# Kernel optimization log

Measured on AMD Instinct MI355X. Metric: run time of the kernel, lower is better.

Reference implementation:

```python
import jax, jax.numpy as jnp
import numpy as np

B, S, E, H = 1, 4096, 768, 12
D = E // H  # head_dim = 64


def setup_inputs() -> dict:
    key = jax.random.key(0)
    ks = jax.random.split(key, 9)
    s = 1.0 / np.sqrt(E)
    return {
        "x": jax.random.normal(ks[0], (B, S, E), dtype=jnp.float32),
        "Wq": jax.random.uniform(ks[1], (E, E), jnp.float32, -s, s),
        "bq": jax.random.uniform(ks[2], (E,), jnp.float32, -s, s),
        "Wk": jax.random.uniform(ks[3], (E, E), jnp.float32, -s, s),
        "bk": jax.random.uniform(ks[4], (E,), jnp.float32, -s, s),
        "Wv": jax.random.uniform(ks[5], (E, E), jnp.float32, -s, s),
        "bv": jax.random.uniform(ks[6], (E,), jnp.float32, -s, s),
        "Wo": jax.random.uniform(ks[7], (E, E), jnp.float32, -s, s),
        "bo": jax.random.uniform(ks[8], (E,), jnp.float32, -s, s),
    }


def reference(x, Wq, bq, Wk, bk, Wv, bv, Wo, bo):
    b, s, e = x.shape
    # QKV projections, split heads -> [b, h, s, d]
    def split(t):
        return t.reshape(b, s, H, D).transpose(0, 2, 1, 3)
    q = split(x @ Wq.T + bq)
    k = split(x @ Wk.T + bk)
    v = split(x @ Wv.T + bv)
    scores = jnp.einsum("bhqd,bhkd->bhqk", q, k) / jnp.sqrt(jnp.float32(D))
    attn = jax.nn.softmax(scores, axis=-1)  # dropout is identity in eval
    out = jnp.einsum("bhqk,bhkd->bhqd", attn, v)
    out = out.transpose(0, 2, 1, 3).reshape(b, s, e)
    return out @ Wo.T + bo
```

## Files before the change

kernel.cpp:

```cpp
#include <hip/hip_runtime.h>
#include <hip/hip_bf16.h>
#include <math.h>

#define SEQ 4096
#define EDIM 768
#define NHEAD 12
#define HDIM 64
#define SE (SEQ * EDIM)
#define WMAT (EDIM * EDIM)
#define QSCALE 0.180336880111f

typedef __attribute__((ext_vector_type(8))) __bf16 bf16x8;
typedef __attribute__((ext_vector_type(4))) float f32x4;
typedef __attribute__((ext_vector_type(16))) float f32x16;
typedef __attribute__((ext_vector_type(8))) unsigned short u16x8;
typedef __attribute__((ext_vector_type(4))) unsigned short u16x4;
typedef unsigned short ushort_t;
typedef unsigned int uint_t;

#define MFMA16(a, b, c) __builtin_amdgcn_mfma_f32_16x16x32_bf16(a, b, c, 0, 0, 0)
#define MFMA32(a, b, c) __builtin_amdgcn_mfma_f32_32x32x16_bf16(a, b, c, 0, 0, 0)
#define GLOAD_LDS16(g, l)                                          \
  __builtin_amdgcn_global_load_lds(                                \
      (const __attribute__((address_space(1))) void*)(g),          \
      (__attribute__((address_space(3))) void*)(l), 16, 0, 0)

__device__ __forceinline__ unsigned short bfbits(float x) {
  return __builtin_bit_cast(unsigned short, (__bf16)x);
}
__device__ __forceinline__ void split1(float x, unsigned short* h,
                                       unsigned short* l) {
  __bf16 hb = (__bf16)x;
  *h = __builtin_bit_cast(unsigned short, hb);
  *l = __builtin_bit_cast(unsigned short, (__bf16)(x - (float)hb));
}
__device__ __forceinline__ bf16x8 ones8() {
  u16x8 u;
#pragma unroll
  for (int e = 0; e < 8; ++e) u[e] = 0x3F80;
  return __builtin_bit_cast(bf16x8, u);
}
__device__ __forceinline__ float exp2_hw(float x) {
  float r;
  asm("v_exp_f32 %0, %1" : "=v"(r) : "v"(x));
  return r;
}
__device__ __forceinline__ uint_t cvtpk(float a, float b) {
  uint_t r;
  asm("v_cvt_pk_bf16_f32 %0, %1, %2" : "=v"(r) : "v"(a), "v"(b));
  return r;
}

__global__ __launch_bounds__(256) void wprep_kernel(
    const float* __restrict__ W0, const float* __restrict__ W1,
    const float* __restrict__ W2, const float* __restrict__ W3,
    ushort_t* __restrict__ WB, ushort_t* __restrict__ WOH,
    ushort_t* __restrict__ WOL) {
  const int m = blockIdx.y;
  const float* src = (m == 0) ? W0 : (m == 1) ? W1 : (m == 2) ? W2 : W3;
  const size_t i = ((size_t)blockIdx.x * 256 + threadIdx.x) * 8;
  float4 a = *(const float4*)(src + i);
  float4 b = *(const float4*)(src + i + 4);
  float fv[8] = {a.x, a.y, a.z, a.w, b.x, b.y, b.z, b.w};
  if (m < 3) {
    u16x8 hh;
#pragma unroll
    for (int e = 0; e < 8; ++e) hh[e] = bfbits(fv[e]);
    *(u16x8*)(WB + (size_t)m * WMAT + i) = hh;
  } else {
    u16x8 hh, ll;
#pragma unroll
    for (int e = 0; e < 8; ++e) {
      unsigned short x, y;
      split1(fv[e], &x, &y);
      hh[e] = x;
      ll[e] = y;
    }
    *(u16x8*)(WOH + i) = hh;
    *(u16x8*)(WOL + i) = ll;
  }
}

__global__ __launch_bounds__(256) void xprep_kernel(
    const float* __restrict__ x, ushort_t* __restrict__ xb) {
  const size_t i = ((size_t)blockIdx.x * 256 + threadIdx.x) * 8;
  float4 a = *(const float4*)(x + i);
  float4 b = *(const float4*)(x + i + 4);
  float fv[8] = {a.x, a.y, a.z, a.w, b.x, b.y, b.z, b.w};
  u16x8 hh;
#pragma unroll
  for (int e = 0; e < 8; ++e) hh[e] = bfbits(fv[e]);
  *(u16x8*)(xb + i) = hh;
}

__global__ __launch_bounds__(256) void qkv_kernel(
    const ushort_t* __restrict__ XB, const ushort_t* __restrict__ WB,
    const float* __restrict__ bq, const float* __restrict__ bk,
    const float* __restrict__ bv, ushort_t* __restrict__ QB,
    ushort_t* __restrict__ KB, ushort_t* __restrict__ VT) {
  __shared__ __align__(16) ushort_t AS[128][32];
  __shared__ __align__(16) ushort_t BS[128][32];

  const int z = blockIdx.z;
  const ushort_t* Bmat = WB + (size_t)z * WMAT;
  const float* bias = (z == 0) ? bq : (z == 1) ? bk : bv;
  ushort_t* outp = (z == 0) ? QB : (z == 1) ? KB : VT;
  const float scale = (z == 0) ? QSCALE : 1.0f;

  const int t = threadIdx.x;
  const int lane = t & 63;
  const int w = t >> 6;
  const int tn = t & 15;
  const int g = (t >> 4) & 3;
  const int wr = w >> 1, wc = w & 1;
  const int m0 = blockIdx.x * 128;
  const int n0 = blockIdx.y * 128;

  f32x4 acc[4][4];
#pragma unroll
  for (int mi = 0; mi < 4; ++mi)
#pragma unroll
    for (int nj = 0; nj < 4; ++nj) acc[mi][nj] = (f32x4){0.f, 0.f, 0.f, 0.f};

  const int crow = lane >> 2;
  const int ccol = (lane & 3) * 8;

  for (int k0 = 0; k0 < EDIM; k0 += 32) {
    __syncthreads();
#pragma unroll
    for (int i = 0; i < 2; ++i) {
      const int ch = w + 4 * i;
      const int row = ch * 16 + crow;
      GLOAD_LDS16(XB + (size_t)(m0 + row) * EDIM + k0 + ccol, &AS[ch * 16][0]);
      GLOAD_LDS16(Bmat + (size_t)(n0 + row) * EDIM + k0 + ccol, &BS[ch * 16][0]);
    }
    __syncthreads();

    bf16x8 ah[4], bh[4];
#pragma unroll
    for (int mi = 0; mi < 4; ++mi)
      ah[mi] = __builtin_bit_cast(
          bf16x8, *(const u16x8*)&AS[wr * 64 + mi * 16 + tn][8 * g]);
#pragma unroll
    for (int nj = 0; nj < 4; ++nj)
      bh[nj] = __builtin_bit_cast(
          bf16x8, *(const u16x8*)&BS[wc * 64 + nj * 16 + tn][8 * g]);
#pragma unroll
    for (int mi = 0; mi < 4; ++mi)
#pragma unroll
      for (int nj = 0; nj < 4; ++nj)
        acc[mi][nj] = MFMA16(ah[mi], bh[nj], acc[mi][nj]);
  }

#pragma unroll
  for (int mi = 0; mi < 4; ++mi) {
    const int rb = m0 + wr * 64 + mi * 16 + 4 * g;
#pragma unroll
    for (int nj = 0; nj < 4; ++nj) {
      const int col = n0 + wc * 64 + nj * 16 + tn;
      const float bb = bias[col];
      if (z == 2) {
        u16x4 pk;
#pragma unroll
        for (int r = 0; r < 4; ++r) pk[r] = bfbits(acc[mi][nj][r] + bb);
        *(u16x4*)(outp + (size_t)col * SEQ + rb) = pk;
      } else {
#pragma unroll
        for (int r = 0; r < 4; ++r)
          outp[(size_t)(rb + r) * EDIM + col] =
              bfbits((acc[mi][nj][r] + bb) * scale);
      }
    }
  }
}

__global__ __launch_bounds__(256) void proj_kernel(
    const ushort_t* __restrict__ Ah, const ushort_t* __restrict__ Al,
    const ushort_t* __restrict__ Bh, const ushort_t* __restrict__ Bl,
    const float* __restrict__ bias, float* __restrict__ outf) {
  __shared__ __align__(16) ushort_t AhS[128][32];
  __shared__ __align__(16) ushort_t AlS[128][32];
  __shared__ __align__(16) ushort_t BhS[128][32];
  __shared__ __align__(16) ushort_t BlS[128][32];

  const int t = threadIdx.x;
  const int lane = t & 63;
  const int w = t >> 6;
  const int tn = t & 15;
  const int g = (t >> 4) & 3;
  const int wr = w >> 1, wc = w & 1;
  const int m0 = blockIdx.x * 128;
  const int n0 = blockIdx.y * 128;

  f32x4 acc[4][4];
#pragma unroll
  for (int mi = 0; mi < 4; ++mi)
#pragma unroll
    for (int nj = 0; nj < 4; ++nj) acc[mi][nj] = (f32x4){0.f, 0.f, 0.f, 0.f};

  const int crow = lane >> 2;
  const int ccol = (lane & 3) * 8;

  for (int k0 = 0; k0 < EDIM; k0 += 32) {
    __syncthreads();
#pragma unroll
    for (int i = 0; i < 2; ++i) {
      const int ch = w + 4 * i;
      const int row = ch * 16 + crow;
      const size_t ga = (size_t)(m0 + row) * EDIM + k0 + ccol;
      const size_t gb = (size_t)(n0 + row) * EDIM + k0 + ccol;
      GLOAD_LDS16(Ah + ga, &AhS[ch * 16][0]);
      GLOAD_LDS16(Al + ga, &AlS[ch * 16][0]);
      GLOAD_LDS16(Bh + gb, &BhS[ch * 16][0]);
      GLOAD_LDS16(Bl + gb, &BlS[ch * 16][0]);
    }
    __syncthreads();

    bf16x8 ah[4], al[4], bh[4], bl[4];
#pragma unroll
    for (int mi = 0; mi < 4; ++mi) {
      ah[mi] = __builtin_bit_cast(
          bf16x8, *(const u16x8*)&AhS[wr * 64 + mi * 16 + tn][8 * g]);
      al[mi] = __builtin_bit_cast(
          bf16x8, *(const u16x8*)&AlS[wr * 64 + mi * 16 + tn][8 * g]);
    }
#pragma unroll
    for (int nj = 0; nj < 4; ++nj) {
      bh[nj] = __builtin_bit_cast(
          bf16x8, *(const u16x8*)&BhS[wc * 64 + nj * 16 + tn][8 * g]);
      bl[nj] = __builtin_bit_cast(
          bf16x8, *(const u16x8*)&BlS[wc * 64 + nj * 16 + tn][8 * g]);
    }
#pragma unroll
    for (int mi = 0; mi < 4; ++mi)
#pragma unroll
      for (int nj = 0; nj < 4; ++nj)
        acc[mi][nj] = MFMA16(ah[mi], bh[nj], acc[mi][nj]);
#pragma unroll
    for (int mi = 0; mi < 4; ++mi)
#pragma unroll
      for (int nj = 0; nj < 4; ++nj)
        acc[mi][nj] = MFMA16(al[mi], bh[nj], acc[mi][nj]);
#pragma unroll
    for (int mi = 0; mi < 4; ++mi)
#pragma unroll
      for (int nj = 0; nj < 4; ++nj)
        acc[mi][nj] = MFMA16(ah[mi], bl[nj], acc[mi][nj]);
  }

#pragma unroll
  for (int mi = 0; mi < 4; ++mi) {
    const int rb = m0 + wr * 64 + mi * 16 + 4 * g;
#pragma unroll
    for (int nj = 0; nj < 4; ++nj) {
      const int col = n0 + wc * 64 + nj * 16 + tn;
      const float bb = bias[col];
#pragma unroll
      for (int r = 0; r < 4; ++r)
        outf[(size_t)(rb + r) * EDIM + col] = acc[mi][nj][r] + bb;
    }
  }
}

__global__ __launch_bounds__(256) void attn_kernel(
    const ushort_t* __restrict__ QB, const ushort_t* __restrict__ KBg,
    const ushort_t* __restrict__ VTg, ushort_t* __restrict__ Ch_g,
    ushort_t* __restrict__ Cl_g) {
  __shared__ __align__(16) ushort_t KS[2][64][64];
  __shared__ __align__(16) ushort_t VS[2][64][64];

  const int t = threadIdx.x;
  const int lane = t & 63;
  const int l31 = lane & 31;
  const int hi = lane >> 5;
  const int wid = t >> 6;
  const int wq = wid & 1;
  const int wk = wid >> 1;
  const int q0 = blockIdx.x * 64;
  const int hoff = blockIdx.y * HDIM;

  bf16x8 qf[4];
  {
    const ushort_t* qp =
        QB + (size_t)(q0 + 32 * wq + l31) * EDIM + hoff + 8 * hi;
#pragma unroll
    for (int s4 = 0; s4 < 4; ++s4)
      qf[s4] = __builtin_bit_cast(bf16x8, *(const u16x8*)(qp + 16 * s4));
  }

  const int srow = lane >> 3;
  const int sxor = ((lane & 7) ^ srow) << 4;

  const bf16x8 ones = ones8();
  f32x16 O0, O1, LS;
#pragma unroll
  for (int r = 0; r < 16; ++r) {
    O0[r] = 0.f;
    O1[r] = 0.f;
    LS[r] = 0.f;
  }

#pragma unroll
  for (int c = 0; c < 2; ++c) {
    const int row = 16 * wid + 8 * c + srow;
    GLOAD_LDS16((const char*)(KBg + (size_t)row * EDIM + hoff) + sxor,
                &KS[0][16 * wid + 8 * c][0]);
    GLOAD_LDS16((const char*)(VTg + (size_t)(hoff + row) * SEQ) + sxor,
                &VS[0][16 * wid + 8 * c][0]);
  }

  const int krow = 32 * wk + l31;
  const int kswz = (krow & 7) << 4;

  for (int it = 0; it < SEQ / 64; ++it) {
    const int buf = it & 1;
    __syncthreads();

    if (it + 1 < SEQ / 64) {
      const int k0n = (it + 1) * 64;
#pragma unroll
      for (int c = 0; c < 2; ++c) {
        const int row = 16 * wid + 8 * c + srow;
        GLOAD_LDS16(
            (const char*)(KBg + (size_t)(k0n + row) * EDIM + hoff) + sxor,
            &KS[buf ^ 1][16 * wid + 8 * c][0]);
        GLOAD_LDS16(
            (const char*)(VTg + (size_t)(hoff + row) * SEQ + k0n) + sxor,
            &VS[buf ^ 1][16 * wid + 8 * c][0]);
      }
    }

    f32x16 s;
#pragma unroll
    for (int r = 0; r < 16; ++r) s[r] = 0.f;
    {
      const char* kb = (const char*)&KS[buf][krow][0];
#pragma unroll
      for (int st = 0; st < 4; ++st) {
        const bf16x8 kf = __builtin_bit_cast(
            bf16x8, *(const u16x8*)(kb + ((32 * st + 16 * hi) ^ kswz)));
        s = MFMA32(kf, qf[st], s);
      }
    }

#pragma unroll
    for (int r = 0; r < 16; ++r) s[r] = exp2_hw(s[r]);

    uint_t w0 = cvtpk(s[0], s[1]), w1 = cvtpk(s[2], s[3]);
    uint_t w2 = cvtpk(s[4], s[5]), w3 = cvtpk(s[6], s[7]);
    uint_t w4 = cvtpk(s[8], s[9]), w5 = cvtpk(s[10], s[11]);
    uint_t w6 = cvtpk(s[12], s[13]), w7 = cvtpk(s[14], s[15]);
    asm("v_permlane32_swap_b32 %0, %1" : "+v"(w0), "+v"(w2));
    asm("v_permlane32_swap_b32 %0, %1" : "+v"(w1), "+v"(w3));
    asm("v_permlane32_swap_b32 %0, %1" : "+v"(w4), "+v"(w6));
    asm("v_permlane32_swap_b32 %0, %1" : "+v"(w5), "+v"(w7));
    const bf16x8 pa0 = __builtin_bit_cast(bf16x8, (uint4){w0, w1, w2, w3});
    const bf16x8 pa1 = __builtin_bit_cast(bf16x8, (uint4){w4, w5, w6, w7});

#pragma unroll
    for (int db = 0; db < 2; ++db) {
      const int vrow = 32 * db + l31;
      const int vswz = (vrow & 7) << 4;
      const char* vb = (const char*)&VS[buf][vrow][0];
      const bf16x8 vf0 = __builtin_bit_cast(
          bf16x8, *(const u16x8*)(vb + ((64 * wk + 16 * hi) ^ vswz)));
      const bf16x8 vf1 = __builtin_bit_cast(
          bf16x8, *(const u16x8*)(vb + ((64 * wk + 32 + 16 * hi) ^ vswz)));
      if (db == 0) {
        O0 = MFMA32(pa0, vf0, O0);
        O0 = MFMA32(pa1, vf1, O0);
      } else {
        O1 = MFMA32(pa0, vf0, O1);
        O1 = MFMA32(pa1, vf1, O1);
      }
    }
    LS = MFMA32(pa0, ones, LS);
    LS = MFMA32(pa1, ones, LS);
  }

  float(*OLt)[64][32] = (float(*)[64][32]) & KS[0][0][0];
  float(*LT)[32] = (float(*)[32]) & VS[0][0][0];

  __syncthreads();
  if (wk == 1) {
#pragma unroll
    for (int j = 0; j < 4; ++j) {
      *(float4*)&OLt[wq][l31][8 * j + 4 * hi] =
          make_float4(O0[4 * j], O0[4 * j + 1], O0[4 * j + 2], O0[4 * j + 3]);
      *(float4*)&OLt[wq][32 + l31][8 * j + 4 * hi] =
          make_float4(O1[4 * j], O1[4 * j + 1], O1[4 * j + 2], O1[4 * j + 3]);
    }
    if (l31 == 0) {
#pragma unroll
      for (int j = 0; j < 4; ++j)
        *(float4*)&LT[wq][8 * j + 4 * hi] = make_float4(
            LS[4 * j], LS[4 * j + 1], LS[4 * j + 2], LS[4 * j + 3]);
    }
  }
  __syncthreads();
  if (wk == 0) {
    float linv[16];
#pragma unroll
    for (int j = 0; j < 4; ++j) {
      const float4 lv = *(const float4*)&LT[wq][8 * j + 4 * hi];
      linv[4 * j + 0] = 1.f / (LS[4 * j + 0] + lv.x);
      linv[4 * j + 1] = 1.f / (LS[4 * j + 1] + lv.y);
      linv[4 * j + 2] = 1.f / (LS[4 * j + 2] + lv.z);
      linv[4 * j + 3] = 1.f / (LS[4 * j + 3] + lv.w);
    }
#pragma unroll
    for (int db = 0; db < 2; ++db) {
      const f32x16 Od = db ? O1 : O0;
#pragma unroll
      for (int j = 0; j < 4; ++j) {
        const float4 ov = *(const float4*)&OLt[wq][32 * db + l31][8 * j + 4 * hi];
        const float vals[4] = {(Od[4 * j + 0] + ov.x) * linv[4 * j + 0],
                               (Od[4 * j + 1] + ov.y) * linv[4 * j + 1],
                               (Od[4 * j + 2] + ov.z) * linv[4 * j + 2],
                               (Od[4 * j + 3] + ov.w) * linv[4 * j + 3]};
#pragma unroll
        for (int e = 0; e < 4; ++e) {
          unsigned short hh, ll;
          split1(vals[e], &hh, &ll);
          const size_t idx =
              (size_t)(q0 + 32 * wq + 8 * j + 4 * hi + e) * EDIM + hoff +
              32 * db + l31;
          Ch_g[idx] = hh;
          Cl_g[idx] = ll;
        }
      }
    }
  }
}

extern "C" void kernel_launch(void* const* d_in, const int* in_sizes, int n_in,
                              void* d_out, int out_size, void* d_ws,
                              size_t ws_size, hipStream_t stream) {
  const float* x  = (const float*)d_in[0];
  const float* Wq = (const float*)d_in[1];
  const float* bq = (const float*)d_in[2];
  const float* Wk = (const float*)d_in[3];
  const float* bk = (const float*)d_in[4];
  const float* Wv = (const float*)d_in[5];
  const float* bv = (const float*)d_in[6];
  const float* Wo = (const float*)d_in[7];
  const float* bo = (const float*)d_in[8];
  float* out = (float*)d_out;

  ushort_t* WB  = (ushort_t*)d_ws;
  ushort_t* WOH = WB + (size_t)3 * WMAT;
  ushort_t* WOL = WOH + (size_t)WMAT;
  ushort_t* XB  = WOL + (size_t)WMAT;
  ushort_t* QB  = XB + (size_t)SE;
  ushort_t* KB  = QB + (size_t)SE;
  ushort_t* VT  = KB + (size_t)SE;
  ushort_t* CH  = VT + (size_t)SE;
  ushort_t* CL  = CH + (size_t)SE;

  dim3 gw(WMAT / 2048, 4);
  wprep_kernel<<<gw, 256, 0, stream>>>(Wq, Wk, Wv, Wo, WB, WOH, WOL);
  xprep_kernel<<<SE / 2048, 256, 0, stream>>>(x, XB);

  dim3 gq(SEQ / 128, EDIM / 128, 3);
  qkv_kernel<<<gq, 256, 0, stream>>>(XB, WB, bq, bk, bv, QB, KB, VT);

  dim3 ga(SEQ / 64, NHEAD);
  attn_kernel<<<ga, 256, 0, stream>>>(QB, KB, VT, CH, CL);

  dim3 go(SEQ / 128, EDIM / 128);
  proj_kernel<<<go, 256, 0, stream>>>(CH, CL, WOH, WOL, bo, out);
}
```

Measured before the change: 186.7 us.

## Split attention key range across two blocks and combine partial outputs

Adds a split-K dimension to the attention grid so each block processes half of the key sequence. The unnormalized partial outputs (as bf16 hi/lo pairs) and partial row sums are written out, and a new combine kernel sums the halves and normalizes. The aim is to double the number of attention blocks (768 to 1536) to fill more CUs and shorten each block's serial loop. The cost is an extra kernel launch plus the extra memory traffic for the partials. The partial buffers reuse workspace regions (XB, WB) that are already consumed by that point.

```diff
diff --git a/kernel.cpp b/kernel.cpp
--- a/kernel.cpp
+++ b/kernel.cpp
@@ -27,6 +27,9 @@
 
 __device__ __forceinline__ unsigned short bfbits(float x) {
   return __builtin_bit_cast(unsigned short, (__bf16)x);
+}
+__device__ __forceinline__ float bf2f(unsigned short u) {
+  return __builtin_bit_cast(float, (uint_t)u << 16);
 }
 __device__ __forceinline__ void split1(float x, unsigned short* h,
                                        unsigned short* l) {
@@ -264,8 +267,9 @@
 
 __global__ __launch_bounds__(256) void attn_kernel(
     const ushort_t* __restrict__ QB, const ushort_t* __restrict__ KBg,
-    const ushort_t* __restrict__ VTg, ushort_t* __restrict__ Ch_g,
-    ushort_t* __restrict__ Cl_g) {
+    const ushort_t* __restrict__ VTg, ushort_t* __restrict__ OH0,
+    ushort_t* __restrict__ OL0, ushort_t* __restrict__ OH1,
+    ushort_t* __restrict__ OL1, float* __restrict__ Lp) {
   __shared__ __align__(16) ushort_t KS[2][64][64];
   __shared__ __align__(16) ushort_t VS[2][64][64];
 
@@ -277,7 +281,12 @@
   const int wq = wid & 1;
   const int wk = wid >> 1;
   const int q0 = blockIdx.x * 64;
-  const int hoff = blockIdx.y * HDIM;
+  const int h = blockIdx.y;
+  const int hoff = h * HDIM;
+  const int kz = blockIdx.z;
+  const int kbase = kz * (SEQ / 2);
+  ushort_t* ohp = kz ? OH1 : OH0;
+  ushort_t* olp = kz ? OL1 : OL0;
 
   bf16x8 qf[4];
   {
@@ -303,21 +312,24 @@
 #pragma unroll
   for (int c = 0; c < 2; ++c) {
     const int row = 16 * wid + 8 * c + srow;
-    GLOAD_LDS16((const char*)(KBg + (size_t)row * EDIM + hoff) + sxor,
-                &KS[0][16 * wid + 8 * c][0]);
-    GLOAD_LDS16((const char*)(VTg + (size_t)(hoff + row) * SEQ) + sxor,
-                &VS[0][16 * wid + 8 * c][0]);
+    GLOAD_LDS16(
+        (const char*)(KBg + (size_t)(kbase + row) * EDIM + hoff) + sxor,
+        &KS[0][16 * wid + 8 * c][0]);
+    GLOAD_LDS16(
+        (const char*)(VTg + (size_t)(hoff + row) * SEQ + kbase) + sxor,
+        &VS[0][16 * wid + 8 * c][0]);
   }
 
   const int krow = 32 * wk + l31;
   const int kswz = (krow & 7) << 4;
-
-  for (int it = 0; it < SEQ / 64; ++it) {
+  const int NT = SEQ / 128;
+
+  for (int it = 0; it < NT; ++it) {
     const int buf = it & 1;
     __syncthreads();
 
-    if (it + 1 < SEQ / 64) {
-      const int k0n = (it + 1) * 64;
+    if (it + 1 < NT) {
+      const int k0n = kbase + (it + 1) * 64;
 #pragma unroll
       for (int c = 0; c < 2; ++c) {
         const int row = 16 * wid + 8 * c + srow;
@@ -399,25 +411,31 @@
   }
   __syncthreads();
   if (wk == 0) {
-    float linv[16];
+    float lt[16];
 #pragma unroll
     for (int j = 0; j < 4; ++j) {
       const float4 lv = *(const float4*)&LT[wq][8 * j + 4 * hi];
-      linv[4 * j + 0] = 1.f / (LS[4 * j + 0] + lv.x);
-      linv[4 * j + 1] = 1.f / (LS[4 * j + 1] + lv.y);
-      linv[4 * j + 2] = 1.f / (LS[4 * j + 2] + lv.z);
-      linv[4 * j + 3] = 1.f / (LS[4 * j + 3] + lv.w);
+      lt[4 * j + 0] = LS[4 * j + 0] + lv.x;
+      lt[4 * j + 1] = LS[4 * j + 1] + lv.y;
+      lt[4 * j + 2] = LS[4 * j + 2] + lv.z;
+      lt[4 * j + 3] = LS[4 * j + 3] + lv.w;
+    }
+    if (l31 == 0) {
+#pragma unroll
+      for (int r = 0; r < 16; ++r) {
+        const int q = (r & 3) + 8 * (r >> 2) + 4 * hi;
+        Lp[(size_t)(kz * NHEAD + h) * SEQ + q0 + 32 * wq + q] = lt[r];
+      }
     }
 #pragma unroll
     for (int db = 0; db < 2; ++db) {
       const f32x16 Od = db ? O1 : O0;
 #pragma unroll
       for (int j = 0; j < 4; ++j) {
-        const float4 ov = *(const float4*)&OLt[wq][32 * db + l31][8 * j + 4 * hi];
-        const float vals[4] = {(Od[4 * j + 0] + ov.x) * linv[4 * j + 0],
-                               (Od[4 * j + 1] + ov.y) * linv[4 * j + 1],
-                               (Od[4 * j + 2] + ov.z) * linv[4 * j + 2],
-                               (Od[4 * j + 3] + ov.w) * linv[4 * j + 3]};
+        const float4 ov =
+            *(const float4*)&OLt[wq][32 * db + l31][8 * j + 4 * hi];
+        const float vals[4] = {Od[4 * j + 0] + ov.x, Od[4 * j + 1] + ov.y,
+                               Od[4 * j + 2] + ov.z, Od[4 * j + 3] + ov.w};
 #pragma unroll
         for (int e = 0; e < 4; ++e) {
           unsigned short hh, ll;
@@ -425,12 +443,40 @@
           const size_t idx =
               (size_t)(q0 + 32 * wq + 8 * j + 4 * hi + e) * EDIM + hoff +
               32 * db + l31;
-          Ch_g[idx] = hh;
-          Cl_g[idx] = ll;
+          ohp[idx] = hh;
+          olp[idx] = ll;
         }
       }
     }
   }
+}
+
+__global__ __launch_bounds__(256) void combine_kernel(
+    ushort_t* __restrict__ OH0, ushort_t* __restrict__ OL0,
+    const ushort_t* __restrict__ OH1, const ushort_t* __restrict__ OL1,
+    const float* __restrict__ Lp) {
+  const size_t i0 = ((size_t)blockIdx.x * 256 + threadIdx.x) * 8;
+  const int q = (int)(i0 / EDIM);
+  const int dc = (int)(i0 % EDIM);
+  const int h = dc >> 6;
+  const float l0 = Lp[(size_t)h * SEQ + q];
+  const float l1 = Lp[(size_t)(NHEAD + h) * SEQ + q];
+  const float inv = 1.f / (l0 + l1);
+  u16x8 a = *(const u16x8*)(OH0 + i0);
+  u16x8 b = *(const u16x8*)(OL0 + i0);
+  u16x8 c = *(const u16x8*)(OH1 + i0);
+  u16x8 d = *(const u16x8*)(OL1 + i0);
+  u16x8 oh, ol;
+#pragma unroll
+  for (int e = 0; e < 8; ++e) {
+    const float v = (bf2f(a[e]) + bf2f(b[e]) + bf2f(c[e]) + bf2f(d[e])) * inv;
+    unsigned short hh, ll;
+    split1(v, &hh, &ll);
+    oh[e] = hh;
+    ol[e] = ll;
+  }
+  *(u16x8*)(OH0 + i0) = oh;
+  *(u16x8*)(OL0 + i0) = ol;
 }
 
 extern "C" void kernel_launch(void* const* d_in, const int* in_sizes, int n_in,
@@ -456,6 +502,9 @@
   ushort_t* VT  = KB + (size_t)SE;
   ushort_t* CH  = VT + (size_t)SE;
   ushort_t* CL  = CH + (size_t)SE;
+  ushort_t* OL1 = CL + (size_t)SE;
+  ushort_t* OH1 = XB;
+  float* Lp = (float*)WB;
 
   dim3 gw(WMAT / 2048, 4);
   wprep_kernel<<<gw, 256, 0, stream>>>(Wq, Wk, Wv, Wo, WB, WOH, WOL);
@@ -464,8 +513,10 @@
   dim3 gq(SEQ / 128, EDIM / 128, 3);
   qkv_kernel<<<gq, 256, 0, stream>>>(XB, WB, bq, bk, bv, QB, KB, VT);
 
-  dim3 ga(SEQ / 64, NHEAD);
-  attn_kernel<<<ga, 256, 0, stream>>>(QB, KB, VT, CH, CL);
+  dim3 ga(SEQ / 64, NHEAD, 2);
+  attn_kernel<<<ga, 256, 0, stream>>>(QB, KB, VT, CH, CL, OH1, OL1, Lp);
+
+  combine_kernel<<<SE / 2048, 256, 0, stream>>>(CH, CL, OH1, OL1, Lp);
 
   dim3 go(SEQ / 128, EDIM / 128);
   proj_kernel<<<go, 256, 0, stream>>>(CH, CL, WOH, WOL, bo, out);
```

New measurement: 173.8 us. 6.9% less time.
